# Optimization experiments

Hardware: AMD Instinct MI355X
Metric: run time of the kernel (lower is better)

## Reference

```python
import math
import jax, jax.numpy as jnp
import numpy as np

B, T_ALL, D = 128, 197, 768
T = T_ALL - 1
ORG, E, DFF, NCLS = 5, 8, 1024, 100
CAP_FACTOR = 1.25
MAX_K = 2  # training=True -> min(2, n_experts)


def setup_inputs() -> dict:
    key = jax.random.key(0)
    ks = jax.random.split(key, 16)
    s = lambda *sh: 0.02
    inp = {
        "tokens": jax.random.normal(ks[0], (B, T_ALL, D), jnp.float32),
        "organ_priors": jax.random.uniform(ks[1], (B, ORG), jnp.float32),
        "router_w": jax.random.normal(ks[2], (D + ORG, E), jnp.float32) * 0.02,
        "router_b": jnp.zeros((E,), jnp.float32),
        "w1": jax.random.normal(ks[3], (E, D, DFF), jnp.float32) * 0.02,
        "b1": jnp.zeros((E, DFF), jnp.float32),
        "w2": jax.random.normal(ks[4], (E, DFF, D), jnp.float32) * 0.02,
        "b2": jnp.zeros((E, D), jnp.float32),
        "ln_g": jnp.ones((D,), jnp.float32),
        "ln_b": jnp.zeros((D,), jnp.float32),
        "cls_w": jax.random.normal(ks[5], (D, NCLS), jnp.float32) * 0.02,
        "cls_b": jnp.zeros((NCLS,), jnp.float32),
        "aux_w": jax.random.normal(ks[6], (D, ORG), jnp.float32) * 0.02,
        "aux_b": jnp.zeros((ORG,), jnp.float32),
    }
    return inp


def switch_moe(flat, flat_prior, router_w, router_b, w1, b1, w2, b2):
    N = flat.shape[0]
    capacity = math.ceil(N / E * CAP_FACTOR)  # static
    logits = jnp.concatenate([flat, flat_prior], axis=-1) @ router_w + router_b  # (N,E)
    probs = jax.nn.softmax(logits, axis=-1)
    entropy = -(probs * jnp.log(probs + 1e-12)).sum(-1)  # (N,)
    topk_vals, topk_idx = jax.lax.top_k(probs, MAX_K)  # (N,K)
    topk_probs = topk_vals / (topk_vals.sum(-1, keepdims=True) + 1e-12)
    # one-hot expert assignment over top-k slots: (N,E)
    sel = jnp.any(topk_idx[:, None, :] == jnp.arange(E)[None, :, None], axis=-1)
    # combine weight per (token, expert): first (unique) matching top-k slot's prob
    w_full = (topk_probs[:, None, :] * (topk_idx[:, None, :] == jnp.arange(E)[None, :, None])).sum(-1)  # (N,E)
    # capacity-limited dispatch: per expert keep top-`capacity` tokens by router prob
    score = jnp.where(sel, probs, -jnp.inf).T  # (E,N)
    top_scores, idx = jax.lax.top_k(score, capacity)  # (E,cap), sorted desc like torch.sort
    valid = jnp.isfinite(top_scores)  # (E,cap)
    gathered = flat[idx]  # (E,cap,D)
    h = jax.nn.gelu(jnp.einsum('ecd,edf->ecf', gathered, w1) + b1[:, None, :], approximate=False)
    out_sel = jnp.einsum('ecf,efd->ecd', h, w2) + b2[:, None, :]  # (E,cap,D)
    w_sel = jnp.take_along_axis(w_full.T, idx, axis=1) * valid  # (E,cap)
    flat_idx = idx.reshape(-1)
    outputs = jnp.zeros_like(flat).at[flat_idx].add((out_sel * w_sel[..., None]).reshape(-1, D))
    processed = jnp.zeros((N,), jnp.float32).at[flat_idx].add(valid.reshape(-1).astype(jnp.float32)) > 0
    outputs = jnp.where(processed[:, None], outputs, flat)
    return outputs, probs, entropy


def reference(tokens, organ_priors, router_w, router_b, w1, b1, w2, b2,
              ln_g, ln_b, cls_w, cls_b, aux_w, aux_b):
    cls = tokens[:, 0, :]                # (B,D)
    patches = tokens[:, 1:, :]           # (B,T,D)
    flat = patches.reshape(B * T, D)
    flat_prior = jnp.broadcast_to(organ_priors[:, None, :], (B, T, ORG)).reshape(B * T, ORG)
    out_flat, probs, entropy = switch_moe(flat, flat_prior, router_w, router_b, w1, b1, w2, b2)
    # cls token passes through MoE untouched (only patches go through switch)
    mu = cls.mean(-1, keepdims=True)
    var = ((cls - mu) ** 2).mean(-1, keepdims=True)
    cls_final = (cls - mu) * jax.lax.rsqrt(var + 1e-5) * ln_g + ln_b
    logits = cls_final @ cls_w + cls_b
    aux_org = cls_final @ aux_w + aux_b
    return logits, aux_org, probs.reshape(B, T, E), entropy.reshape(B, T)
```

## Files before the change

### kernel.cpp

```cpp
#include <hip/hip_runtime.h>
#include <hip/hip_bf16.h>
#include <math.h>

#define NB     128
#define NT_ALL 197
#define NT     196
#define ND     768
#define NORG   5
#define NE     8
#define NCLS   100
#define NCOL   105
#define NTOK   (NB * NT)
#define KB     24
#define KHALF  12

#define RBLKS  784
#define CBLKS  256

typedef short  bf16x8 __attribute__((ext_vector_type(8)));
typedef float  f32x4  __attribute__((ext_vector_type(4)));


__global__ __launch_bounds__(256, 3) void fused_kernel(
    const float* __restrict__ tokens,
    const float* __restrict__ priors,
    const float* __restrict__ rw,
    const float* __restrict__ rbias,
    const float* __restrict__ ln_g, const float* __restrict__ ln_b,
    const float* __restrict__ cls_w,
    const float* __restrict__ cls_b,
    const float* __restrict__ aux_w,
    const float* __restrict__ aux_b,
    float* __restrict__ out_logits,
    float* __restrict__ out_aux,
    float* __restrict__ probs_out,
    float* __restrict__ ent_out)
{
    const int t = threadIdx.x;

    if (blockIdx.x < RBLKS) {
        __shared__ __align__(16) __hip_bfloat16 s_a[KB * 4 * 16 * 8];
        __shared__ float s_pl[2][NE];
        __shared__ __align__(16) float s_acc[2][64][4];

        const int wid  = t >> 6;
        const int lane = t & 63;
        const int pair = wid >> 1;
        const int half = wid & 1;
        const int tt   = lane & 15;
        const int g    = lane >> 4;
        const int tok0 = blockIdx.x * 32;
        const int token = tok0 + pair * 16 + tt;
        const int b  = token / NT;
        const float* xp = tokens + ((size_t)b * NT_ALL + 1 + (token - b * NT)) * ND
                          + half * (KHALF * 32) + g * 8;

        float4 x[2 * KHALF];
#pragma unroll
        for (int i = 0; i < KHALF; ++i) {
            x[2 * i]     = *reinterpret_cast<const float4*>(xp + i * 32);
            x[2 * i + 1] = *reinterpret_cast<const float4*>(xp + i * 32 + 4);
        }
        __builtin_amdgcn_sched_barrier(0);

        {
            bf16x8 z = {0, 0, 0, 0, 0, 0, 0, 0};
            bf16x8* p = (bf16x8*)s_a;
            for (int i = t; i < KB * 4 * 8; i += 256)
                p[(i >> 3) * 16 + 8 + (i & 7)] = z;
        }
        for (int i = t; i < ND * NE; i += 256) {
            const int k = i >> 3, e = i & 7;
            const int kb = k >> 5, gg = (k >> 3) & 3, j = k & 7;
            s_a[(((kb * 4 + gg) * 16) + e) * 8 + j] = __float2bfloat16(rw[i]);
        }
        const int b0 = tok0 / NT;
        const int b1 = (tok0 + 31) / NT;
        if (t < 16) {
            const int e = t & 7, which = t >> 3;
            const int bb = which ? b1 : b0;
            float a = rbias[e];
#pragma unroll
            for (int o = 0; o < NORG; ++o)
                a = fmaf(priors[bb * NORG + o], rw[(ND + o) * NE + e], a);
            s_pl[which][e] = a;
        }
        __syncthreads();

        const bf16x8* s_a8 = (const bf16x8*)s_a + (half * KHALF * 4 + g) * 16 + tt;
        f32x4 acc0 = {0.f, 0.f, 0.f, 0.f};
        f32x4 acc1 = {0.f, 0.f, 0.f, 0.f};

#pragma unroll
        for (int kb = 0; kb < KHALF; ++kb) {
            const float4 x0 = x[2 * kb];
            const float4 x1 = x[2 * kb + 1];
            union { bf16x8 v; __hip_bfloat16 h[8]; } u;
            u.h[0] = __float2bfloat16(x0.x);
            u.h[1] = __float2bfloat16(x0.y);
            u.h[2] = __float2bfloat16(x0.z);
            u.h[3] = __float2bfloat16(x0.w);
            u.h[4] = __float2bfloat16(x1.x);
            u.h[5] = __float2bfloat16(x1.y);
            u.h[6] = __float2bfloat16(x1.z);
            u.h[7] = __float2bfloat16(x1.w);
            const bf16x8 af = s_a8[kb * 64];
            if (kb & 1)
                acc1 = __builtin_amdgcn_mfma_f32_16x16x32_bf16(af, u.v, acc1, 0, 0, 0);
            else
                acc0 = __builtin_amdgcn_mfma_f32_16x16x32_bf16(af, u.v, acc0, 0, 0, 0);
        }
        f32x4 acc = acc0 + acc1;

        if (half == 1)
            *reinterpret_cast<f32x4*>(&s_acc[pair][lane][0]) = acc;
        __syncthreads();

        if (half == 0) {
            acc += *reinterpret_cast<const f32x4*>(&s_acc[pair][lane][0]);

            const float p0 = __shfl_xor(acc[0], 16, 64);
            const float p1 = __shfl_xor(acc[1], 16, 64);
            const float p2 = __shfl_xor(acc[2], 16, 64);
            const float p3 = __shfl_xor(acc[3], 16, 64);

            if (lane < 16) {
                float lg[NE] = {acc[0], acc[1], acc[2], acc[3], p0, p1, p2, p3};
                const int bsel = (b == b0) ? 0 : 1;
#pragma unroll
                for (int e = 0; e < NE; ++e) lg[e] += s_pl[bsel][e];

                float m = lg[0];
#pragma unroll
                for (int e = 1; e < NE; ++e) m = fmaxf(m, lg[e]);
                float S = 0.f, dd = 0.f;
#pragma unroll
                for (int e = 0; e < NE; ++e) {
                    const float l = lg[e] - m;
                    const float p = __expf(l);
                    lg[e] = p;
                    S += p;
                    dd = fmaf(p, l, dd);
                }
                const float inv = 1.f / S;
                const float ent = __logf(S) - dd * inv;

                float4 q0 = {lg[0] * inv, lg[1] * inv, lg[2] * inv, lg[3] * inv};
                float4 q1 = {lg[4] * inv, lg[5] * inv, lg[6] * inv, lg[7] * inv};
                *reinterpret_cast<float4*>(probs_out + (size_t)token * NE)     = q0;
                *reinterpret_cast<float4*>(probs_out + (size_t)token * NE + 4) = q1;
                ent_out[token] = ent;
            }
        }
    } else {
        const int cb   = blockIdx.x - RBLKS;
        const int b    = cb >> 1;
        const int half = cb & 1;
        const int lane = t & 63;
        const int wv   = t >> 6;

        __shared__ __align__(16) float s_x[ND];
        __shared__ float s_red[4];
        __shared__ float s_part[4][65];

        const float* xp = tokens + (size_t)b * NT_ALL * ND;

        float sum = 0.f;
        for (int i = t; i < ND; i += 256) { float v = xp[i]; s_x[i] = v; sum += v; }
#pragma unroll
        for (int off = 32; off; off >>= 1) sum += __shfl_xor(sum, off, 64);
        if (lane == 0) s_red[wv] = sum;
        __syncthreads();
        const float mu = (s_red[0] + s_red[1] + s_red[2] + s_red[3]) * (1.f / ND);
        __syncthreads();

        float sq = 0.f;
        for (int i = t; i < ND; i += 256) { float d = s_x[i] - mu; sq += d * d; }
#pragma unroll
        for (int off = 32; off; off >>= 1) sq += __shfl_xor(sq, off, 64);
        if (lane == 0) s_red[wv] = sq;
        __syncthreads();
        const float var  = (s_red[0] + s_red[1] + s_red[2] + s_red[3]) * (1.f / ND);
        const float rstd = rsqrtf(var + 1e-5f);
        __syncthreads();

        for (int i = t; i < ND; i += 256)
            s_x[i] = (s_x[i] - mu) * rstd * ln_g[i] + ln_b[i];
        __syncthreads();

        const int c = half * 64 + lane;
        const float* wp; int st;
        if (c < NCLS)      { wp = cls_w + c;          st = NCLS; }
        else if (c < NCOL) { wp = aux_w + (c - NCLS); st = NORG; }
        else               { wp = aux_w;              st = NORG; }

        const int d0 = wv * 192;
        const float* w = wp + (size_t)d0 * st;
        const int st2 = 2 * st, st3 = 3 * st, st4 = 4 * st;
        float a0 = 0.f, a1 = 0.f, a2 = 0.f, a3 = 0.f;
#pragma unroll 8
        for (int j = 0; j < 192; j += 4) {
            const float4 x4 = *reinterpret_cast<const float4*>(&s_x[d0 + j]);
            a0 = fmaf(x4.x, w[0],   a0);
            a1 = fmaf(x4.y, w[st],  a1);
            a2 = fmaf(x4.z, w[st2], a2);
            a3 = fmaf(x4.w, w[st3], a3);
            w += st4;
        }
        s_part[wv][lane] = (a0 + a1) + (a2 + a3);
        __syncthreads();

        if (t < 64) {
            float r = s_part[0][t] + s_part[1][t] + s_part[2][t] + s_part[3][t];
            const int cc = half * 64 + t;
            if (cc < NCLS)
                out_logits[b * NCLS + cc] = r + cls_b[cc];
            else if (cc < NCOL)
                out_aux[b * NORG + (cc - NCLS)] = r + aux_b[cc - NCLS];
        }
    }
}

extern "C" void kernel_launch(void* const* d_in, const int* in_sizes, int n_in,
                              void* d_out, int out_size, void* d_ws, size_t ws_size,
                              hipStream_t stream) {
    const float* tokens = (const float*)d_in[0];
    const float* priors = (const float*)d_in[1];
    const float* rw     = (const float*)d_in[2];
    const float* rbias  = (const float*)d_in[3];
    const float* ln_g   = (const float*)d_in[8];
    const float* ln_b   = (const float*)d_in[9];
    const float* cls_w  = (const float*)d_in[10];
    const float* cls_b  = (const float*)d_in[11];
    const float* aux_w  = (const float*)d_in[12];
    const float* aux_b  = (const float*)d_in[13];

    float* out = (float*)d_out;
    float* out_logits = out;
    float* out_aux    = out + NB * NCLS;
    float* out_probs  = out + NB * NCLS + NB * NORG;
    float* out_ent    = out + NB * NCLS + NB * NORG + (size_t)NTOK * NE;

    fused_kernel<<<RBLKS + CBLKS, 256, 0, stream>>>(
        tokens, priors, rw, rbias, ln_g, ln_b, cls_w, cls_b, aux_w, aux_b,
        out_logits, out_aux, out_probs, out_ent);
}
```

Baseline: 27.66 us.

## Stage router token tile in LDS as bf16 with coalesced loads

Router blocks now load their 32-token tile with fully coalesced float4 loads across the whole block, convert to bf16 and store into a padded LDS buffer. The MFMA loop then reads bf16x8 fragments from LDS instead of holding 24 float4 values in registers per thread. Shared memory for both block roles is merged into a union, and launch bounds raise the occupancy target from 3 to 4. The aim is better global access patterns and lower register pressure, in exchange for about 50KB of LDS per block, which may cap residency.

```diff
diff --git a/kernel.cpp b/kernel.cpp
--- a/kernel.cpp
+++ b/kernel.cpp
@@ -13,6 +13,7 @@
 #define NTOK   (NB * NT)
 #define KB     24
 #define KHALF  12
+#define XROW   776
 
 #define RBLKS  784
 #define CBLKS  256
@@ -21,7 +22,19 @@
 typedef float  f32x4  __attribute__((ext_vector_type(4)));
 
 
-__global__ __launch_bounds__(256, 3) void fused_kernel(
+struct SharedRouter {
+    __hip_bfloat16 x[32 * XROW];
+    __hip_bfloat16 a[KB * 4 * 16 * 8];
+    float pl[2][NE];
+    float acc[2][64][4];
+};
+struct SharedCls {
+    float x[ND];
+    float red[4];
+    float part[4][65];
+};
+
+__global__ __launch_bounds__(256, 4) void fused_kernel(
     const float* __restrict__ tokens,
     const float* __restrict__ priors,
     const float* __restrict__ rw,
@@ -36,12 +49,51 @@
     float* __restrict__ probs_out,
     float* __restrict__ ent_out)
 {
+    __shared__ union { SharedRouter r; SharedCls c; } sm;
     const int t = threadIdx.x;
 
     if (blockIdx.x < RBLKS) {
-        __shared__ __align__(16) __hip_bfloat16 s_a[KB * 4 * 16 * 8];
-        __shared__ float s_pl[2][NE];
-        __shared__ __align__(16) float s_acc[2][64][4];
+        const int tok0 = blockIdx.x * 32;
+
+#pragma unroll 6
+        for (int i = t; i < 32 * ND / 4; i += 256) {
+            const int tok = i / 192;
+            const int k   = (i - tok * 192) * 4;
+            const int gt  = tok0 + tok;
+            const int b   = gt / NT;
+            const float4 v = *reinterpret_cast<const float4*>(
+                tokens + (size_t)(gt + b + 1) * ND + k);
+            union { __hip_bfloat16 h[4]; ushort4 u; } pk;
+            pk.h[0] = __float2bfloat16(v.x);
+            pk.h[1] = __float2bfloat16(v.y);
+            pk.h[2] = __float2bfloat16(v.z);
+            pk.h[3] = __float2bfloat16(v.w);
+            *reinterpret_cast<ushort4*>(&sm.r.x[tok * XROW + k]) = pk.u;
+        }
+
+        {
+            bf16x8 z = {0, 0, 0, 0, 0, 0, 0, 0};
+            bf16x8* p = (bf16x8*)sm.r.a;
+            for (int i = t; i < KB * 4 * 8; i += 256)
+                p[(i >> 3) * 16 + 8 + (i & 7)] = z;
+        }
+        for (int i = t; i < ND * NE; i += 256) {
+            const int k = i >> 3, e = i & 7;
+            const int kb = k >> 5, gg = (k >> 3) & 3, j = k & 7;
+            sm.r.a[(((kb * 4 + gg) * 16) + e) * 8 + j] = __float2bfloat16(rw[i]);
+        }
+        const int b0 = tok0 / NT;
+        const int b1 = (tok0 + 31) / NT;
+        if (t < 16) {
+            const int e = t & 7, which = t >> 3;
+            const int bb = which ? b1 : b0;
+            float a = rbias[e];
+#pragma unroll
+            for (int o = 0; o < NORG; ++o)
+                a = fmaf(priors[bb * NORG + o], rw[(ND + o) * NE + e], a);
+            sm.r.pl[which][e] = a;
+        }
+        __syncthreads();
 
         const int wid  = t >> 6;
         const int lane = t & 63;
@@ -49,75 +101,33 @@
         const int half = wid & 1;
         const int tt   = lane & 15;
         const int g    = lane >> 4;
-        const int tok0 = blockIdx.x * 32;
         const int token = tok0 + pair * 16 + tt;
         const int b  = token / NT;
-        const float* xp = tokens + ((size_t)b * NT_ALL + 1 + (token - b * NT)) * ND
-                          + half * (KHALF * 32) + g * 8;
-
-        float4 x[2 * KHALF];
-#pragma unroll
-        for (int i = 0; i < KHALF; ++i) {
-            x[2 * i]     = *reinterpret_cast<const float4*>(xp + i * 32);
-            x[2 * i + 1] = *reinterpret_cast<const float4*>(xp + i * 32 + 4);
-        }
-        __builtin_amdgcn_sched_barrier(0);
-
-        {
-            bf16x8 z = {0, 0, 0, 0, 0, 0, 0, 0};
-            bf16x8* p = (bf16x8*)s_a;
-            for (int i = t; i < KB * 4 * 8; i += 256)
-                p[(i >> 3) * 16 + 8 + (i & 7)] = z;
-        }
-        for (int i = t; i < ND * NE; i += 256) {
-            const int k = i >> 3, e = i & 7;
-            const int kb = k >> 5, gg = (k >> 3) & 3, j = k & 7;
-            s_a[(((kb * 4 + gg) * 16) + e) * 8 + j] = __float2bfloat16(rw[i]);
-        }
-        const int b0 = tok0 / NT;
-        const int b1 = (tok0 + 31) / NT;
-        if (t < 16) {
-            const int e = t & 7, which = t >> 3;
-            const int bb = which ? b1 : b0;
-            float a = rbias[e];
-#pragma unroll
-            for (int o = 0; o < NORG; ++o)
-                a = fmaf(priors[bb * NORG + o], rw[(ND + o) * NE + e], a);
-            s_pl[which][e] = a;
-        }
-        __syncthreads();
-
-        const bf16x8* s_a8 = (const bf16x8*)s_a + (half * KHALF * 4 + g) * 16 + tt;
+
+        const bf16x8* s_a8 =
+            (const bf16x8*)sm.r.a + (half * KHALF * 4 + g) * 16 + tt;
+        const __hip_bfloat16* xrow =
+            sm.r.x + (pair * 16 + tt) * XROW + half * (KHALF * 32) + g * 8;
+
         f32x4 acc0 = {0.f, 0.f, 0.f, 0.f};
         f32x4 acc1 = {0.f, 0.f, 0.f, 0.f};
-
 #pragma unroll
         for (int kb = 0; kb < KHALF; ++kb) {
-            const float4 x0 = x[2 * kb];
-            const float4 x1 = x[2 * kb + 1];
-            union { bf16x8 v; __hip_bfloat16 h[8]; } u;
-            u.h[0] = __float2bfloat16(x0.x);
-            u.h[1] = __float2bfloat16(x0.y);
-            u.h[2] = __float2bfloat16(x0.z);
-            u.h[3] = __float2bfloat16(x0.w);
-            u.h[4] = __float2bfloat16(x1.x);
-            u.h[5] = __float2bfloat16(x1.y);
-            u.h[6] = __float2bfloat16(x1.z);
-            u.h[7] = __float2bfloat16(x1.w);
+            const bf16x8 xf = *reinterpret_cast<const bf16x8*>(xrow + kb * 32);
             const bf16x8 af = s_a8[kb * 64];
             if (kb & 1)
-                acc1 = __builtin_amdgcn_mfma_f32_16x16x32_bf16(af, u.v, acc1, 0, 0, 0);
+                acc1 = __builtin_amdgcn_mfma_f32_16x16x32_bf16(af, xf, acc1, 0, 0, 0);
             else
-                acc0 = __builtin_amdgcn_mfma_f32_16x16x32_bf16(af, u.v, acc0, 0, 0, 0);
+                acc0 = __builtin_amdgcn_mfma_f32_16x16x32_bf16(af, xf, acc0, 0, 0, 0);
         }
         f32x4 acc = acc0 + acc1;
 
         if (half == 1)
-            *reinterpret_cast<f32x4*>(&s_acc[pair][lane][0]) = acc;
+            *reinterpret_cast<f32x4*>(&sm.r.acc[pair][lane][0]) = acc;
         __syncthreads();
 
         if (half == 0) {
-            acc += *reinterpret_cast<const f32x4*>(&s_acc[pair][lane][0]);
+            acc += *reinterpret_cast<const f32x4*>(&sm.r.acc[pair][lane][0]);
 
             const float p0 = __shfl_xor(acc[0], 16, 64);
             const float p1 = __shfl_xor(acc[1], 16, 64);
@@ -128,7 +138,7 @@
                 float lg[NE] = {acc[0], acc[1], acc[2], acc[3], p0, p1, p2, p3};
                 const int bsel = (b == b0) ? 0 : 1;
 #pragma unroll
-                for (int e = 0; e < NE; ++e) lg[e] += s_pl[bsel][e];
+                for (int e = 0; e < NE; ++e) lg[e] += sm.r.pl[bsel][e];
 
                 float m = lg[0];
 #pragma unroll
@@ -159,33 +169,29 @@
         const int lane = t & 63;
         const int wv   = t >> 6;
 
-        __shared__ __align__(16) float s_x[ND];
-        __shared__ float s_red[4];
-        __shared__ float s_part[4][65];
-
         const float* xp = tokens + (size_t)b * NT_ALL * ND;
 
         float sum = 0.f;
-        for (int i = t; i < ND; i += 256) { float v = xp[i]; s_x[i] = v; sum += v; }
+        for (int i = t; i < ND; i += 256) { float v = xp[i]; sm.c.x[i] = v; sum += v; }
 #pragma unroll
         for (int off = 32; off; off >>= 1) sum += __shfl_xor(sum, off, 64);
-        if (lane == 0) s_red[wv] = sum;
-        __syncthreads();
-        const float mu = (s_red[0] + s_red[1] + s_red[2] + s_red[3]) * (1.f / ND);
+        if (lane == 0) sm.c.red[wv] = sum;
+        __syncthreads();
+        const float mu = (sm.c.red[0] + sm.c.red[1] + sm.c.red[2] + sm.c.red[3]) * (1.f / ND);
         __syncthreads();
 
         float sq = 0.f;
-        for (int i = t; i < ND; i += 256) { float d = s_x[i] - mu; sq += d * d; }
+        for (int i = t; i < ND; i += 256) { float d = sm.c.x[i] - mu; sq += d * d; }
 #pragma unroll
         for (int off = 32; off; off >>= 1) sq += __shfl_xor(sq, off, 64);
-        if (lane == 0) s_red[wv] = sq;
-        __syncthreads();
-        const float var  = (s_red[0] + s_red[1] + s_red[2] + s_red[3]) * (1.f / ND);
+        if (lane == 0) sm.c.red[wv] = sq;
+        __syncthreads();
+        const float var  = (sm.c.red[0] + sm.c.red[1] + sm.c.red[2] + sm.c.red[3]) * (1.f / ND);
         const float rstd = rsqrtf(var + 1e-5f);
         __syncthreads();
 
         for (int i = t; i < ND; i += 256)
-            s_x[i] = (s_x[i] - mu) * rstd * ln_g[i] + ln_b[i];
+            sm.c.x[i] = (sm.c.x[i] - mu) * rstd * ln_g[i] + ln_b[i];
         __syncthreads();
 
         const int c = half * 64 + lane;
@@ -200,18 +206,18 @@
         float a0 = 0.f, a1 = 0.f, a2 = 0.f, a3 = 0.f;
 #pragma unroll 8
         for (int j = 0; j < 192; j += 4) {
-            const float4 x4 = *reinterpret_cast<const float4*>(&s_x[d0 + j]);
+            const float4 x4 = *reinterpret_cast<const float4*>(&sm.c.x[d0 + j]);
             a0 = fmaf(x4.x, w[0],   a0);
             a1 = fmaf(x4.y, w[st],  a1);
             a2 = fmaf(x4.z, w[st2], a2);
             a3 = fmaf(x4.w, w[st3], a3);
             w += st4;
         }
-        s_part[wv][lane] = (a0 + a1) + (a2 + a3);
+        sm.c.part[wv][lane] = (a0 + a1) + (a2 + a3);
         __syncthreads();
 
         if (t < 64) {
-            float r = s_part[0][t] + s_part[1][t] + s_part[2][t] + s_part[3][t];
+            float r = sm.c.part[0][t] + sm.c.part[1][t] + sm.c.part[2][t] + sm.c.part[3][t];
             const int cc = half * 64 + t;
             if (cc < NCLS)
                 out_logits[b * NCLS + cc] = r + cls_b[cc];
```

Result: faster. 26.87 us (-2.9%).
